# Kernel optimization log

Hardware: AMD Instinct MI355X
Metric: run time of the kernel (lower is better)

Reference implementation:

```python
import jax, jax.numpy as jnp
import numpy as np

EPS = 1e-5


def spline_conv(x, src, dst, pseudo, W, root, bias, num_nodes, K=5):
    """Degree-1 open B-spline conv (torch_spline_conv semantics), mean aggregation.
    W: [kernel_total, Cin, Cout]. kernel_total==1 means trivial basis (kernel_size=1)."""
    E = src.shape[0]
    Cin = x.shape[1]
    KT = W.shape[0]
    x_j = x[src]                                            # [E, Cin] edge gather
    deg = jax.ops.segment_sum(jnp.ones((E,), x.dtype), dst, num_segments=num_nodes)
    deg = jnp.maximum(deg, 1.0)
    if KT == 1:
        agg = jax.ops.segment_sum(x_j, dst, num_segments=num_nodes)
        out = (agg / deg[:, None]) @ W[0]
    else:
        v = pseudo * (K - 1)                                # open spline: v in [0, K-1]
        f = jnp.clip(jnp.floor(v), 0.0, K - 2)
        frac = v - f                                        # [E, 2]
        fi = f.astype(jnp.int32)
        # bucket basis-weighted source features by (kernel_index, dst) then one dense einsum
        h = jnp.zeros((KT * num_nodes, Cin), x.dtype)
        for s0 in (0, 1):
            for s1 in (0, 1):
                b0 = frac[:, 0] if s0 else 1.0 - frac[:, 0]
                b1 = frac[:, 1] if s1 else 1.0 - frac[:, 1]
                basis = b0 * b1                             # [E]
                wi = (fi[:, 0] + s0) + K * (fi[:, 1] + s1)  # [E] kernel index in [0,25)
                seg = wi * num_nodes + dst
                h = h + jax.ops.segment_sum(basis[:, None] * x_j, seg,
                                            num_segments=KT * num_nodes)
        agg = jnp.einsum('knc,kco->no', h.reshape(KT, num_nodes, Cin), W)
        out = agg / deg[:, None]
    return out + x @ root + bias


def batch_norm(x, gamma, beta):
    m = x.mean(axis=0)
    var = jnp.mean((x - m) ** 2, axis=0)
    return gamma * (x - m) * jax.lax.rsqrt(var + EPS) + beta


def setup_inputs() -> dict:
    key = jax.random.key(0)
    ks = jax.random.split(key, 8)
    N, E, Cin, Cout = 50000, 800000, 32, 64
    x = jax.random.normal(ks[0], (N, Cin), jnp.float32)
    edge_index = jax.random.randint(ks[1], (2, E), 0, N, jnp.int32)
    edge_attr = jax.random.uniform(ks[2], (E, 2), jnp.float32)
    s = 0.1
    return {
        'x': x, 'edge_index': edge_index, 'edge_attr': edge_attr,
        'w1': jax.random.normal(ks[3], (25, Cin, Cout), jnp.float32) * s,
        'r1': jax.random.normal(ks[4], (Cin, Cout), jnp.float32) * s,
        'b1': jnp.zeros((Cout,), jnp.float32),
        'g1': jnp.ones((Cout,), jnp.float32),
        'beta1': jnp.zeros((Cout,), jnp.float32),
        'w2': jax.random.normal(ks[5], (25, Cout, Cout), jnp.float32) * s,
        'r2': jax.random.normal(ks[6], (Cout, Cout), jnp.float32) * s,
        'b2': jnp.zeros((Cout,), jnp.float32),
        'g2': jnp.ones((Cout,), jnp.float32),
        'beta2': jnp.zeros((Cout,), jnp.float32),
        'ws': jax.random.normal(ks[7], (1, Cin, Cout), jnp.float32) * s,
        'rs': jax.random.normal(jax.random.fold_in(key, 99), (Cin, Cout), jnp.float32) * s,
        'bs': jnp.zeros((Cout,), jnp.float32),
        'gs': jnp.ones((Cout,), jnp.float32),
        'betas': jnp.zeros((Cout,), jnp.float32),
    }


def reference(x, edge_index, edge_attr, w1, r1, b1, g1, beta1,
              w2, r2, b2, g2, beta2, ws, rs, bs, gs, betas):
    N = x.shape[0]
    src, dst = edge_index[0], edge_index[1]
    h = jax.nn.elu(batch_norm(spline_conv(x, src, dst, edge_attr, w1, r1, b1, N), g1, beta1))
    left = batch_norm(spline_conv(h, src, dst, edge_attr, w2, r2, b2, N), g2, beta2)
    short = batch_norm(spline_conv(x, src, dst, edge_attr, ws, rs, bs, N), gs, betas)
    return jax.nn.elu(left + short)
```

## Files before the change

kernel.cpp:

```cpp
#include <hip/hip_runtime.h>

#define NN 50000
#define NE 800000
#define DBINS 1024

typedef __attribute__((ext_vector_type(8))) short bf16x8;
typedef __attribute__((ext_vector_type(4))) float f32x4;
typedef __attribute__((ext_vector_type(2))) float f32x2;

__device__ __forceinline__ unsigned short f2bf(float f) {
    union { float f; unsigned u; } v; v.f = f;
    unsigned r = v.u + 0x7FFFu + ((v.u >> 16) & 1u);
    return (unsigned short)(r >> 16);
}

__device__ __forceinline__ int4 ld_ep2(const int4* ep, unsigned idx, int which) {
    return *(const int4*)((const char*)ep + (size_t)(idx * 32u + (unsigned)which * 16u));
}
__device__ __forceinline__ unsigned ld_xu(const unsigned* X, unsigned byteoff) {
    return *(const unsigned*)((const char*)X + (size_t)byteoff);
}

__device__ __forceinline__ f32x2 unpack2(unsigned u) {
    union { unsigned u; float f; } a, b;
    a.u = u << 16;
    b.u = u & 0xFFFF0000u;
    return f32x2{a.f, b.f};
}

__device__ __forceinline__ f32x2 pk_mul_hib(f32x2 w, f32x2 x) {
    f32x2 d;
    asm("v_pk_mul_f32 %0, %1, %2 op_sel:[1,0] op_sel_hi:[1,1]"
        : "=v"(d) : "v"(w), "v"(x));
    return d;
}
__device__ __forceinline__ void pk_fma_lob(f32x2& h, f32x2 w, f32x2 t) {
    asm("v_pk_fma_f32 %0, %1, %2, %0 op_sel:[0,0,0] op_sel_hi:[0,1,1]"
        : "+v"(h) : "v"(w), "v"(t));
}

__device__ __forceinline__ int us_idx(int kk, int r, int m) {
    return kk*544 + (r >> 3)*136 + m*8 + (r & 7);
}

template<bool HS>
__device__ __forceinline__ void edge_acc2(f32x2* h, f32x2& hs,
                                          const int4& pa, const int4& pb, f32x2 x) {
    f32x2 wxy[5];
    wxy[0] = unpack2((unsigned)pa.y);
    wxy[1] = unpack2((unsigned)pa.z);
    wxy[2] = unpack2((unsigned)pa.w);
    wxy[3] = unpack2((unsigned)pb.x);
    wxy[4] = unpack2((unsigned)pb.y);
    if (HS) hs += x;
#pragma unroll
    for (int r1 = 0; r1 < 5; ++r1) {
        f32x2 ty = pk_mul_hib(wxy[r1], x);
#pragma unroll
        for (int r0 = 0; r0 < 5; ++r0)
            pk_fma_lob(h[r1*5 + r0], wxy[r0], ty);
    }
}

__device__ __forceinline__ float eh_reduce(f32x2 v, int eh, int stride) {
    float mine  = eh ? v.y : v.x;
    float other = eh ? v.x : v.y;
    return mine + __shfl_xor(other, stride);
}

__global__ __launch_bounds__(256) void k_zero(int* degi, int* cur, float* stats,
                                              int* dcnt, int* dcur,
                                              unsigned* xz, unsigned* hz) {
    int i = blockIdx.x*256 + threadIdx.x;
    int stride = gridDim.x*256;
    for (int j = i; j < NN; j += stride) { degi[j] = 0; cur[j] = 0; }
    if (i < 384) stats[i] = 0.f;
    if (i < DBINS) { dcnt[i] = 0; dcur[i] = 0; }
    if (i < 16) xz[i] = 0u;
    if (i < 32) hz[i] = 0u;
}

__global__ __launch_bounds__(256) void k_hist(const int* __restrict__ dst, int* degi) {
    int e = blockIdx.x*256 + threadIdx.x;
    if (e < NE) atomicAdd(&degi[dst[e]], 1);
}

__global__ __launch_bounds__(256) void k_scan_block(const int* __restrict__ degi,
                                                    int* off, int* bsum) {
    __shared__ int sh[256];
    int t = threadIdx.x;
    int base = blockIdx.x * 1024;
    int v[4]; int s = 0;
#pragma unroll
    for (int j = 0; j < 4; j++) {
        int idx = base + t*4 + j;
        v[j] = (idx < NN) ? ((degi[idx] + 3) & ~3) : 0;
        s += v[j];
    }
    sh[t] = s; __syncthreads();
    for (int ofs = 1; ofs < 256; ofs <<= 1) {
        int x = (t >= ofs) ? sh[t - ofs] : 0;
        __syncthreads();
        sh[t] += x;
        __syncthreads();
    }
    int ex = sh[t] - s;
#pragma unroll
    for (int j = 0; j < 4; j++) {
        int idx = base + t*4 + j;
        if (idx < NN) off[idx] = ex;
        ex += v[j];
    }
    if (t == 255) bsum[blockIdx.x] = sh[255];
}

__global__ __launch_bounds__(256) void k_scan_top(const int* __restrict__ bsum,
                                                  int* bpre, int nb) {
    __shared__ int sh[256];
    int t = threadIdx.x;
    int s = (t < nb) ? bsum[t] : 0;
    sh[t] = s; __syncthreads();
    for (int ofs = 1; ofs < 256; ofs <<= 1) {
        int x = (t >= ofs) ? sh[t - ofs] : 0;
        __syncthreads();
        sh[t] += x;
        __syncthreads();
    }
    if (t < nb) bpre[t] = sh[t] - s;
}

__global__ __launch_bounds__(256) void k_scan_add(int* off, const int* __restrict__ bpre,
                                                  const int* __restrict__ degi) {
    int i = blockIdx.x*256 + threadIdx.x;
    if (i < NN) {
        int v = off[i] + bpre[i >> 10];
        off[i] = v;
        if (i == NN - 1) off[NN] = v + ((degi[i] + 3) & ~3);
    }
}

__global__ __launch_bounds__(256) void k_dhist(const int* __restrict__ degi, int* dcnt) {
    __shared__ int lh[DBINS];
    int t = threadIdx.x;
#pragma unroll
    for (int j = 0; j < DBINS/256; ++j) lh[t + 256*j] = 0;
    __syncthreads();
    int n = blockIdx.x*256 + t;
    if (n < NN) atomicAdd(&lh[min(degi[n], DBINS-1)], 1);
    __syncthreads();
#pragma unroll
    for (int j = 0; j < DBINS/256; ++j) {
        int b = t + 256*j;
        if (lh[b]) atomicAdd(&dcnt[b], lh[b]);
    }
}

__global__ __launch_bounds__(256) void k_dscan(const int* __restrict__ dcnt, int* dbase) {
    __shared__ int sh[256];
    int t = threadIdx.x;
    int v[4]; int s = 0;
#pragma unroll
    for (int j = 0; j < 4; j++) { v[j] = dcnt[t*4 + j]; s += v[j]; }
    sh[t] = s; __syncthreads();
    for (int ofs = 1; ofs < 256; ofs <<= 1) {
        int x = (t >= ofs) ? sh[t - ofs] : 0;
        __syncthreads();
        sh[t] += x;
        __syncthreads();
    }
    int ex = sh[t] - s;
#pragma unroll
    for (int j = 0; j < 4; j++) { dbase[t*4 + j] = ex; ex += v[j]; }
}

__global__ __launch_bounds__(256) void k_pscatter(const int* __restrict__ degi,
                                                  const int* __restrict__ dbase,
                                                  int* dcur, int* perm) {
    __shared__ int lh[DBINS];
    __shared__ int lb[DBINS];
    int t = threadIdx.x;
#pragma unroll
    for (int j = 0; j < DBINS/256; ++j) lh[t + 256*j] = 0;
    __syncthreads();
    int n = blockIdx.x*256 + t;
    int d = 0, lr = 0;
    bool act = (n < NN);
    if (act) {
        d = min(degi[n], DBINS-1);
        lr = atomicAdd(&lh[d], 1);
    }
    __syncthreads();
#pragma unroll
    for (int j = 0; j < DBINS/256; ++j) {
        int b = t + 256*j;
        int c = lh[b];
        lb[b] = c ? atomicAdd(&dcur[b], c) : 0;
    }
    __syncthreads();
    if (act) perm[dbase[d] + lb[d] + lr] = n;
}

__global__ __launch_bounds__(256) void k_scatter(const int* __restrict__ src,
                                                 const int* __restrict__ dst,
                                                 const float* __restrict__ ea,
                                                 const int* __restrict__ off, int* cur,
                                                 int4* __restrict__ ep) {
    int e = blockIdx.x*256 + threadIdx.x;
    if (e >= NE) return;
    int d = dst[e];
    int p = off[d] + atomicAdd(&cur[d], 1);
    float v0 = ea[2*e]     * 4.f;
    float v1 = ea[2*e + 1] * 4.f;
    unsigned w[5];
#pragma unroll
    for (int r = 0; r < 5; ++r) {
        float wx = fmaxf(1.f - fabsf(v0 - (float)r), 0.f);
        float wy = fmaxf(1.f - fabsf(v1 - (float)r), 0.f);
        w[r] = (unsigned)f2bf(wx) | ((unsigned)f2bf(wy) << 16);
    }
    ep[2*p]     = make_int4(src[e], (int)w[0], (int)w[1], (int)w[2]);
    ep[2*p + 1] = make_int4((int)w[3], (int)w[4], 0, 0);
}

__global__ __launch_bounds__(256) void k_pad(const int* __restrict__ off,
                                             const int* __restrict__ degi,
                                             int4* __restrict__ ep) {
    int n = blockIdx.x*256 + threadIdx.x;
    if (n >= NN) return;
    int base = off[n] + degi[n];
    int end  = off[n + 1];
    for (int p = base; p < end; ++p) {
        ep[2*p]     = make_int4(NN, 0, 0, 0);
        ep[2*p + 1] = make_int4(0, 0, 0, 0);
    }
}

__global__ __launch_bounds__(256) void k_xbf(const float* __restrict__ x,
                                             unsigned short* __restrict__ xb) {
    int i = blockIdx.x*256 + threadIdx.x;
    if (i >= NN*8) return;
    float4 v = ((const float4*)x)[i];
    uint2 pk;
    pk.x = (unsigned)f2bf(v.x) | ((unsigned)f2bf(v.y) << 16);
    pk.y = (unsigned)f2bf(v.z) | ((unsigned)f2bf(v.w) << 16);
    ((uint2*)xb)[i] = pk;
}

__global__ __launch_bounds__(256) void k_wprep(const float* __restrict__ W,
                                               const float* __restrict__ root,
                                               int KTC, unsigned short* Wb) {
    int tid = blockIdx.x*256 + threadIdx.x;
    int lane = tid & 63, cot = (tid >> 6) & 3, kk = tid >> 8;
    int co = 16*cot + (lane & 15);
    int kbase = kk*32 + ((lane >> 4) * 8);
    union { unsigned short s[8]; uint4 v; } u;
#pragma unroll
    for (int j = 0; j < 8; j++) {
        int k = kbase + j;
        float val = (k < KTC) ? W[(size_t)k*64 + co] : root[(size_t)(k - KTC)*64 + co];
        u.s[j] = f2bf(val);
    }
    *(uint4*)(Wb + (size_t)tid * 8) = u.v;
}

__global__ __launch_bounds__(512, 4) void k_conv1s(
        const unsigned* __restrict__ Xbf,
        const int* __restrict__ off,
        const int* __restrict__ degi,
        const int4* __restrict__ ep,
        const int* __restrict__ perm,
        const unsigned short* __restrict__ Wb1,
        const unsigned short* __restrict__ WbS,
        const float* __restrict__ b1,
        const float* __restrict__ bs,
        float* __restrict__ agg1,
        float* __restrict__ aggS) {
    __shared__ __align__(16) unsigned short hb[28*544];
    const int t = threadIdx.x;
    const int g = t >> 5;
    const int q = t & 31;
    const int chp = q & 15;
    const int eh = q >> 4;
    const int n0 = blockIdx.x * 16;
    const int n = perm[n0 + g];

    f32x2 h[25], hs = {0.f, 0.f};
#pragma unroll
    for (int i = 0; i < 25; ++i) h[i] = f32x2{0.f, 0.f};

    const int ebeg = off[n], eend = off[n + 1];
    const float rdeg = 1.f / (float)max(degi[n], 1);

    for (int i = ebeg; i < eend; i += 4) {
        const unsigned i0 = (unsigned)(i + eh), i1 = (unsigned)(i + 2 + eh);
        int4 a0 = ld_ep2(ep, i0, 0), b0 = ld_ep2(ep, i0, 1);
        int4 a1 = ld_ep2(ep, i1, 0), b1 = ld_ep2(ep, i1, 1);
        unsigned u0 = ld_xu(Xbf, (unsigned)a0.x * 64u + (unsigned)chp * 4u);
        unsigned u1 = ld_xu(Xbf, (unsigned)a1.x * 64u + (unsigned)chp * 4u);
        edge_acc2<true>(h, hs, a0, b0, unpack2(u0));
        edge_acc2<true>(h, hs, a1, b1, unpack2(u1));
    }

    const int c = 2*chp + eh;
    const int bw = us_idx(0, c, g);
#pragma unroll
    for (int wi = 0; wi < 25; ++wi)
        hb[wi*544 + bw] = f2bf(eh_reduce(h[wi], eh, 16) * rdeg);
    hb[26*544 + bw] = f2bf(eh_reduce(hs, eh, 16) * rdeg);
    {
        unsigned ux = Xbf[(unsigned)n * 16u + (unsigned)chp];
        unsigned short xb = eh ? (unsigned short)(ux >> 16)
                               : (unsigned short)(ux & 0xFFFFu);
        hb[25*544 + bw] = xb;
        hb[27*544 + bw] = xb;
    }
    __syncthreads();

    const int lane = t & 63, w = t >> 6;
    const int m = lane & 15, qq = lane >> 4;
    const int co = (w & 3)*16 + m;
    const int4 pn = ((const int4*)perm)[(n0 >> 2) + qq];
    const int prow[4] = {pn.x, pn.y, pn.z, pn.w};
    if (w < 4) {
        f32x4 acc = {0.f, 0.f, 0.f, 0.f};
        for (int kk = 0; kk < 26; ++kk) {
            bf16x8 av = *(const bf16x8*)&hb[kk*544 + qq*136 + m*8];
            bf16x8 bv = *(const bf16x8*)(Wb1 + (size_t)((kk*4 + w)*64 + lane) * 8);
            acc = __builtin_amdgcn_mfma_f32_16x16x32_bf16(av, bv, acc, 0, 0, 0);
        }
        const float bb = b1[co];
#pragma unroll
        for (int r = 0; r < 4; ++r)
            agg1[(size_t)prow[r]*64 + co] = acc[r] + bb;
    } else {
        f32x4 accs = {0.f, 0.f, 0.f, 0.f};
#pragma unroll
        for (int s = 0; s < 2; ++s) {
            bf16x8 av = *(const bf16x8*)&hb[(26 + s)*544 + qq*136 + m*8];
            bf16x8 bv = *(const bf16x8*)(WbS + (size_t)((s*4 + (w & 3))*64 + lane) * 8);
            accs = __builtin_amdgcn_mfma_f32_16x16x32_bf16(av, bv, accs, 0, 0, 0);
        }
        const float bb = bs[co];
#pragma unroll
        for (int r = 0; r < 4; ++r)
            aggS[(size_t)prow[r]*64 + co] = accs[r] + bb;
    }
}

__global__ __launch_bounds__(512, 4) void k_conv2(
        const unsigned* __restrict__ Xbf,
        const int* __restrict__ off,
        const int* __restrict__ degi,
        const int4* __restrict__ ep,
        const int* __restrict__ perm,
        const unsigned short* __restrict__ Wb2,
        const float* __restrict__ b2,
        float* __restrict__ agg) {
    __shared__ __align__(16) unsigned short hb[52*544];
    const int t = threadIdx.x, lane = t & 63, w = t >> 6;
    const int n0 = blockIdx.x * 16;
    const int chp = lane & 31, eh = lane >> 5;
    const int c = 2*chp + eh;
    const int kh = c >> 5, r = c & 31;

#pragma unroll
    for (int nn = 0; nn < 2; ++nn) {
        const int g = 2*w + nn;
        const int n = perm[n0 + g];
        f32x2 h[25]; f32x2 hsd = {0.f, 0.f};
#pragma unroll
        for (int i = 0; i < 25; ++i) h[i] = f32x2{0.f, 0.f};

        const int ebeg = off[n], eend = off[n + 1];
        const float rdeg = 1.f / (float)max(degi[n], 1);

        for (int i = ebeg; i < eend; i += 4) {
            const unsigned i0 = (unsigned)(i + eh), i1 = (unsigned)(i + 2 + eh);
            int4 a0 = ld_ep2(ep, i0, 0), b0 = ld_ep2(ep, i0, 1);
            int4 a1 = ld_ep2(ep, i1, 0), b1 = ld_ep2(ep, i1, 1);
            unsigned u0 = ld_xu(Xbf, (unsigned)a0.x * 128u + (unsigned)chp * 4u);
            unsigned u1 = ld_xu(Xbf, (unsigned)a1.x * 128u + (unsigned)chp * 4u);
            edge_acc2<false>(h, hsd, a0, b0, unpack2(u0));
            edge_acc2<false>(h, hsd, a1, b1, unpack2(u1));
        }

        const int bw = us_idx(0, r, g);
#pragma unroll
        for (int wi = 0; wi < 25; ++wi)
            hb[(wi*2 + kh)*544 + bw] = f2bf(eh_reduce(h[wi], eh, 32) * rdeg);
        {
            unsigned ux = Xbf[(unsigned)n * 32u + (unsigned)chp];
            hb[(50 + kh)*544 + bw] =
                (unsigned short)(eh ? (ux >> 16) : (ux & 0xFFFFu));
        }
    }
    __syncthreads();

    if (w >= 4) return;

    const int m = lane & 15, qq = lane >> 4;
    const int4 pn = ((const int4*)perm)[(n0 >> 2) + qq];
    const int prow[4] = {pn.x, pn.y, pn.z, pn.w};
    f32x4 acc = {0.f, 0.f, 0.f, 0.f};
    for (int kk = 0; kk < 52; ++kk) {
        bf16x8 av = *(const bf16x8*)&hb[kk*544 + qq*136 + m*8];
        bf16x8 bv = *(const bf16x8*)(Wb2 + (size_t)((kk*4 + w)*64 + lane) * 8);
        acc = __builtin_amdgcn_mfma_f32_16x16x32_bf16(av, bv, acc, 0, 0, 0);
    }
    const int co = w*16 + m;
    const float bb = b2[co];
#pragma unroll
    for (int rr = 0; rr < 4; ++rr)
        agg[(size_t)prow[rr]*64 + co] = acc[rr] + bb;
}

__global__ __launch_bounds__(256) void k_bnstats(const float* __restrict__ agg, float* stats) {
    __shared__ float sh0[256], sh1[256];
    int t = threadIdx.x;
    float s = 0.f, ss = 0.f;
    int stride = gridDim.x * 256;
    for (int i = blockIdx.x*256 + t; i < NN*64; i += stride) {
        float v = agg[i];
        s += v; ss += v*v;
    }
    sh0[t] = s; sh1[t] = ss;
    __syncthreads();
    if (t < 64) {
        float a = sh0[t] + sh0[t+64] + sh0[t+128] + sh0[t+192];
        float b = sh1[t] + sh1[t+64] + sh1[t+128] + sh1[t+192];
        atomicAdd(&stats[t], a);
        atomicAdd(&stats[64 + t], b);
    }
}

__device__ __forceinline__ float eluf(float u) { return u > 0.f ? u : expm1f(u); }

__global__ __launch_bounds__(256) void k_bn_elu(const float* __restrict__ agg,
                                                const float* __restrict__ stats,
                                                const float* __restrict__ gamma,
                                                const float* __restrict__ beta,
                                                unsigned short* __restrict__ outb) {
    int i = blockIdx.x*256 + threadIdx.x;
    if (i >= NN*16) return;
    float4 v = ((const float4*)agg)[i];
    float r[4] = {v.x, v.y, v.z, v.w};
    int c0 = (i << 2) & 63;
#pragma unroll
    for (int j = 0; j < 4; j++) {
        int c = c0 + j;
        float mu = stats[c] * (1.f/NN);
        float var = stats[64 + c] * (1.f/NN) - mu*mu;
        float sc = gamma[c] * rsqrtf(fmaxf(var, 0.f) + 1e-5f);
        r[j] = eluf((r[j] - mu)*sc + beta[c]);
    }
    uint2 pk;
    pk.x = (unsigned)f2bf(r[0]) | ((unsigned)f2bf(r[1]) << 16);
    pk.y = (unsigned)f2bf(r[2]) | ((unsigned)f2bf(r[3]) << 16);
    ((uint2*)outb)[i] = pk;
}

__global__ __launch_bounds__(256) void k_bn_final(const float* __restrict__ a2,
                                                  const float* __restrict__ st2,
                                                  const float* __restrict__ g2,
                                                  const float* __restrict__ be2,
                                                  const float* __restrict__ as,
                                                  const float* __restrict__ sts,
                                                  const float* __restrict__ gs,
                                                  const float* __restrict__ bes,
                                                  float* __restrict__ out) {
    int i = blockIdx.x*256 + threadIdx.x;
    if (i >= NN*16) return;
    float4 v2 = ((const float4*)a2)[i];
    float4 vs = ((const float4*)as)[i];
    float r2v[4] = {v2.x, v2.y, v2.z, v2.w};
    float rsv[4] = {vs.x, vs.y, vs.z, vs.w};
    float o[4];
    int c0 = (i << 2) & 63;
#pragma unroll
    for (int j = 0; j < 4; j++) {
        int c = c0 + j;
        float mu2 = st2[c] * (1.f/NN);
        float var2 = st2[64 + c] * (1.f/NN) - mu2*mu2;
        float sc2 = g2[c] * rsqrtf(fmaxf(var2, 0.f) + 1e-5f);
        float mus = sts[c] * (1.f/NN);
        float vars = sts[64 + c] * (1.f/NN) - mus*mus;
        float scs = gs[c] * rsqrtf(fmaxf(vars, 0.f) + 1e-5f);
        float u = (r2v[j] - mu2)*sc2 + be2[c] + (rsv[j] - mus)*scs + bes[c];
        o[j] = eluf(u);
    }
    ((float4*)out)[i] = make_float4(o[0], o[1], o[2], o[3]);
}

extern "C" void kernel_launch(void* const* d_in, const int* in_sizes, int n_in,
                              void* d_out, int out_size, void* d_ws, size_t ws_size,
                              hipStream_t stream) {
    const float* x   = (const float*)d_in[0];
    const int*   ei  = (const int*)d_in[1];
    const float* ea  = (const float*)d_in[2];
    const float* w1  = (const float*)d_in[3];
    const float* r1  = (const float*)d_in[4];
    const float* b1  = (const float*)d_in[5];
    const float* g1  = (const float*)d_in[6];
    const float* be1 = (const float*)d_in[7];
    const float* w2  = (const float*)d_in[8];
    const float* r2  = (const float*)d_in[9];
    const float* b2  = (const float*)d_in[10];
    const float* g2  = (const float*)d_in[11];
    const float* be2 = (const float*)d_in[12];
    const float* wsN = (const float*)d_in[13];
    const float* rs  = (const float*)d_in[14];
    const float* bs  = (const float*)d_in[15];
    const float* gs  = (const float*)d_in[16];
    const float* bes = (const float*)d_in[17];
    const int* srcp = ei;
    const int* dstp = ei + NE;

    char* wsb = (char*)d_ws;
    size_t o = 0;
    auto alloc = [&](size_t bytes) -> char* {
        char* p = wsb + o;
        o += (bytes + 255) & ~(size_t)255;
        return p;
    };
    int*    degi    = (int*)   alloc((size_t)NN * 4);
    int*    cur     = (int*)   alloc((size_t)NN * 4);
    int*    off     = (int*)   alloc((size_t)(NN + 1) * 4);
    int*    bsum    = (int*)   alloc(256 * 4);
    int*    bpre    = (int*)   alloc(256 * 4);
    int*    dcnt    = (int*)   alloc(DBINS * 4);
    int*    dcur    = (int*)   alloc(DBINS * 4);
    int*    dbase   = (int*)   alloc(DBINS * 4);
    int*    perm    = (int*)   alloc((size_t)NN * 4);
    int4*   ep      = (int4*)  alloc(((size_t)NE + 3*NN + 64) * 32);
    unsigned short* Wb1 = (unsigned short*)alloc(26 * 4096);
    unsigned short* WbS = (unsigned short*)alloc(2 * 4096);
    unsigned short* Wb2 = (unsigned short*)alloc(52 * 4096);
    float*  agg1    = (float*) alloc((size_t)NN * 64 * 4);
    float*  aggS    = (float*) alloc((size_t)NN * 64 * 4);
    unsigned short* h1bf = (unsigned short*)alloc((size_t)(NN + 1) * 64 * 2);
    unsigned short* xbf  = (unsigned short*)alloc((size_t)(NN + 1) * 32 * 2);
    float*  stats   = (float*) alloc(384 * 4);
    (void)ws_size; (void)in_sizes; (void)n_in; (void)out_size;

    float* out = (float*)d_out;

    k_zero<<<196, 256, 0, stream>>>(degi, cur, stats, dcnt, dcur,
                                    (unsigned*)(xbf + (size_t)NN * 32),
                                    (unsigned*)(h1bf + (size_t)NN * 64));
    k_hist<<<3125, 256, 0, stream>>>(dstp, degi);
    k_scan_block<<<49, 256, 0, stream>>>(degi, off, bsum);
    k_scan_top<<<1, 256, 0, stream>>>(bsum, bpre, 49);
    k_scan_add<<<196, 256, 0, stream>>>(off, bpre, degi);
    k_dhist<<<196, 256, 0, stream>>>(degi, dcnt);
    k_dscan<<<1, 256, 0, stream>>>(dcnt, dbase);
    k_pscatter<<<196, 256, 0, stream>>>(degi, dbase, dcur, perm);
    k_scatter<<<3125, 256, 0, stream>>>(srcp, dstp, ea, off, cur, ep);
    k_pad<<<196, 256, 0, stream>>>(off, degi, ep);

    k_xbf<<<1563, 256, 0, stream>>>(x, xbf);
    k_wprep<<<26, 256, 0, stream>>>(w1, r1, 800, Wb1);
    k_wprep<<<2, 256, 0, stream>>>(wsN, rs, 32, WbS);
    k_wprep<<<52, 256, 0, stream>>>(w2, r2, 1600, Wb2);

    k_conv1s<<<3125, 512, 0, stream>>>((const unsigned*)xbf, off, degi, ep, perm,
                                       Wb1, WbS, b1, bs, agg1, aggS);
    k_bnstats<<<256, 256, 0, stream>>>(agg1, stats);
    k_bn_elu<<<3125, 256, 0, stream>>>(agg1, stats, g1, be1, h1bf);

    k_conv2<<<3125, 512, 0, stream>>>((const unsigned*)h1bf, off, degi, ep, perm,
                                      Wb2, b2, agg1);
    k_bnstats<<<256, 256, 0, stream>>>(agg1, stats + 128);
    k_bnstats<<<256, 256, 0, stream>>>(aggS, stats + 256);
    k_bn_final<<<3125, 256, 0, stream>>>(agg1, stats + 128, g2, be2,
                                         aggS, stats + 256, gs, bes, out);
}
```

Baseline: 458.4 us.

## Fuse small prep kernels and shrink conv2 blocks to eight nodes

Cuts the launch count by merging the two top-level scans into one two-block kernel, folding padding into the permutation scatter, combining the x bf16 conversion with all weight prep, and merging the two final BN stat passes. conv2 also moves to 256-thread blocks covering 8 nodes, with a smaller LDS tile and twice as many blocks, to raise occupancy. The MFMA stage in conv2 now computes 16 rows and keeps only 8, so half of that matrix work is wasted.

```diff
diff --git a/kernel.cpp b/kernel.cpp
--- a/kernel.cpp
+++ b/kernel.cpp
@@ -41,6 +41,9 @@
 
 __device__ __forceinline__ int us_idx(int kk, int r, int m) {
     return kk*544 + (r >> 3)*136 + m*8 + (r & 7);
+}
+__device__ __forceinline__ int us8_idx(int kk, int r, int m) {
+    return kk*272 + (r >> 3)*68 + m*8 + (r & 7);
 }
 
 template<bool HS>
@@ -114,19 +117,53 @@
     if (t == 255) bsum[blockIdx.x] = sh[255];
 }
 
-__global__ __launch_bounds__(256) void k_scan_top(const int* __restrict__ bsum,
-                                                  int* bpre, int nb) {
+__global__ __launch_bounds__(256) void k_dhist(const int* __restrict__ degi, int* dcnt) {
+    __shared__ int lh[DBINS];
+    int t = threadIdx.x;
+#pragma unroll
+    for (int j = 0; j < DBINS/256; ++j) lh[t + 256*j] = 0;
+    __syncthreads();
+    int n = blockIdx.x*256 + t;
+    if (n < NN) atomicAdd(&lh[min(degi[n], DBINS-1)], 1);
+    __syncthreads();
+#pragma unroll
+    for (int j = 0; j < DBINS/256; ++j) {
+        int b = t + 256*j;
+        if (lh[b]) atomicAdd(&dcnt[b], lh[b]);
+    }
+}
+
+__global__ __launch_bounds__(256) void k_topscan(const int* __restrict__ bsum,
+                                                 int* bpre, int nb,
+                                                 const int* __restrict__ dcnt,
+                                                 int* dbase) {
     __shared__ int sh[256];
     int t = threadIdx.x;
-    int s = (t < nb) ? bsum[t] : 0;
-    sh[t] = s; __syncthreads();
-    for (int ofs = 1; ofs < 256; ofs <<= 1) {
-        int x = (t >= ofs) ? sh[t - ofs] : 0;
-        __syncthreads();
-        sh[t] += x;
-        __syncthreads();
-    }
-    if (t < nb) bpre[t] = sh[t] - s;
+    if (blockIdx.x == 0) {
+        int s = (t < nb) ? bsum[t] : 0;
+        sh[t] = s; __syncthreads();
+        for (int ofs = 1; ofs < 256; ofs <<= 1) {
+            int x = (t >= ofs) ? sh[t - ofs] : 0;
+            __syncthreads();
+            sh[t] += x;
+            __syncthreads();
+        }
+        if (t < nb) bpre[t] = sh[t] - s;
+    } else {
+        int v[4]; int s = 0;
+#pragma unroll
+        for (int j = 0; j < 4; j++) { v[j] = dcnt[t*4 + j]; s += v[j]; }
+        sh[t] = s; __syncthreads();
+        for (int ofs = 1; ofs < 256; ofs <<= 1) {
+            int x = (t >= ofs) ? sh[t - ofs] : 0;
+            __syncthreads();
+            sh[t] += x;
+            __syncthreads();
+        }
+        int ex = sh[t] - s;
+#pragma unroll
+        for (int j = 0; j < 4; j++) { dbase[t*4 + j] = ex; ex += v[j]; }
+    }
 }
 
 __global__ __launch_bounds__(256) void k_scan_add(int* off, const int* __restrict__ bpre,
@@ -139,43 +176,11 @@
     }
 }
 
-__global__ __launch_bounds__(256) void k_dhist(const int* __restrict__ degi, int* dcnt) {
-    __shared__ int lh[DBINS];
-    int t = threadIdx.x;
-#pragma unroll
-    for (int j = 0; j < DBINS/256; ++j) lh[t + 256*j] = 0;
-    __syncthreads();
-    int n = blockIdx.x*256 + t;
-    if (n < NN) atomicAdd(&lh[min(degi[n], DBINS-1)], 1);
-    __syncthreads();
-#pragma unroll
-    for (int j = 0; j < DBINS/256; ++j) {
-        int b = t + 256*j;
-        if (lh[b]) atomicAdd(&dcnt[b], lh[b]);
-    }
-}
-
-__global__ __launch_bounds__(256) void k_dscan(const int* __restrict__ dcnt, int* dbase) {
-    __shared__ int sh[256];
-    int t = threadIdx.x;
-    int v[4]; int s = 0;
-#pragma unroll
-    for (int j = 0; j < 4; j++) { v[j] = dcnt[t*4 + j]; s += v[j]; }
-    sh[t] = s; __syncthreads();
-    for (int ofs = 1; ofs < 256; ofs <<= 1) {
-        int x = (t >= ofs) ? sh[t - ofs] : 0;
-        __syncthreads();
-        sh[t] += x;
-        __syncthreads();
-    }
-    int ex = sh[t] - s;
-#pragma unroll
-    for (int j = 0; j < 4; j++) { dbase[t*4 + j] = ex; ex += v[j]; }
-}
-
-__global__ __launch_bounds__(256) void k_pscatter(const int* __restrict__ degi,
-                                                  const int* __restrict__ dbase,
-                                                  int* dcur, int* perm) {
+__global__ __launch_bounds__(256) void k_pscatter_pad(const int* __restrict__ degi,
+                                                      const int* __restrict__ dbase,
+                                                      int* dcur, int* perm,
+                                                      const int* __restrict__ off,
+                                                      int4* __restrict__ ep) {
     __shared__ int lh[DBINS];
     __shared__ int lb[DBINS];
     int t = threadIdx.x;
@@ -197,7 +202,15 @@
         lb[b] = c ? atomicAdd(&dcur[b], c) : 0;
     }
     __syncthreads();
-    if (act) perm[dbase[d] + lb[d] + lr] = n;
+    if (act) {
+        perm[dbase[d] + lb[d] + lr] = n;
+        int base = off[n] + degi[n];
+        int end  = off[n + 1];
+        for (int p = base; p < end; ++p) {
+            ep[2*p]     = make_int4(NN, 0, 0, 0);
+            ep[2*p + 1] = make_int4(0, 0, 0, 0);
+        }
+    }
 }
 
 __global__ __launch_bounds__(256) void k_scatter(const int* __restrict__ src,
@@ -222,34 +235,8 @@
     ep[2*p + 1] = make_int4((int)w[3], (int)w[4], 0, 0);
 }
 
-__global__ __launch_bounds__(256) void k_pad(const int* __restrict__ off,
-                                             const int* __restrict__ degi,
-                                             int4* __restrict__ ep) {
-    int n = blockIdx.x*256 + threadIdx.x;
-    if (n >= NN) return;
-    int base = off[n] + degi[n];
-    int end  = off[n + 1];
-    for (int p = base; p < end; ++p) {
-        ep[2*p]     = make_int4(NN, 0, 0, 0);
-        ep[2*p + 1] = make_int4(0, 0, 0, 0);
-    }
-}
-
-__global__ __launch_bounds__(256) void k_xbf(const float* __restrict__ x,
-                                             unsigned short* __restrict__ xb) {
-    int i = blockIdx.x*256 + threadIdx.x;
-    if (i >= NN*8) return;
-    float4 v = ((const float4*)x)[i];
-    uint2 pk;
-    pk.x = (unsigned)f2bf(v.x) | ((unsigned)f2bf(v.y) << 16);
-    pk.y = (unsigned)f2bf(v.z) | ((unsigned)f2bf(v.w) << 16);
-    ((uint2*)xb)[i] = pk;
-}
-
-__global__ __launch_bounds__(256) void k_wprep(const float* __restrict__ W,
-                                               const float* __restrict__ root,
-                                               int KTC, unsigned short* Wb) {
-    int tid = blockIdx.x*256 + threadIdx.x;
+__device__ __forceinline__ void wprep_body(int tid, const float* W, const float* root,
+                                           int KTC, unsigned short* Wb) {
     int lane = tid & 63, cot = (tid >> 6) & 3, kk = tid >> 8;
     int co = 16*cot + (lane & 15);
     int kbase = kk*32 + ((lane >> 4) * 8);
@@ -261,6 +248,35 @@
         u.s[j] = f2bf(val);
     }
     *(uint4*)(Wb + (size_t)tid * 8) = u.v;
+}
+
+__global__ __launch_bounds__(256) void k_prep(const float* __restrict__ x,
+                                              unsigned short* __restrict__ xb,
+                                              const float* __restrict__ w1,
+                                              const float* __restrict__ r1,
+                                              unsigned short* Wb1,
+                                              const float* __restrict__ wsN,
+                                              const float* __restrict__ rs,
+                                              unsigned short* WbS,
+                                              const float* __restrict__ w2,
+                                              const float* __restrict__ r2,
+                                              unsigned short* Wb2) {
+    int b = blockIdx.x, t = threadIdx.x;
+    if (b < 1563) {
+        int i = b*256 + t;
+        if (i >= NN*8) return;
+        float4 v = ((const float4*)x)[i];
+        uint2 pk;
+        pk.x = (unsigned)f2bf(v.x) | ((unsigned)f2bf(v.y) << 16);
+        pk.y = (unsigned)f2bf(v.z) | ((unsigned)f2bf(v.w) << 16);
+        ((uint2*)xb)[i] = pk;
+    } else if (b < 1589) {
+        wprep_body((b - 1563)*256 + t, w1, r1, 800, Wb1);
+    } else if (b < 1591) {
+        wprep_body((b - 1589)*256 + t, wsN, rs, 32, WbS);
+    } else {
+        wprep_body((b - 1591)*256 + t, w2, r2, 1600, Wb2);
+    }
 }
 
 __global__ __launch_bounds__(512, 4) void k_conv1s(
@@ -347,7 +363,7 @@
     }
 }
 
-__global__ __launch_bounds__(512, 4) void k_conv2(
+__global__ __launch_bounds__(256, 5) void k_conv2(
         const unsigned* __restrict__ Xbf,
         const int* __restrict__ off,
         const int* __restrict__ degi,
@@ -356,9 +372,9 @@
         const unsigned short* __restrict__ Wb2,
         const float* __restrict__ b2,
         float* __restrict__ agg) {
-    __shared__ __align__(16) unsigned short hb[52*544];
+    __shared__ __align__(16) unsigned short hb[52*272 + 256];
     const int t = threadIdx.x, lane = t & 63, w = t >> 6;
-    const int n0 = blockIdx.x * 16;
+    const int n0 = blockIdx.x * 8;
     const int chp = lane & 31, eh = lane >> 5;
     const int c = 2*chp + eh;
     const int kh = c >> 5, r = c & 31;
@@ -384,34 +400,34 @@
             edge_acc2<false>(h, hsd, a1, b1, unpack2(u1));
         }
 
-        const int bw = us_idx(0, r, g);
+        const int bw = us8_idx(0, r, g);
 #pragma unroll
         for (int wi = 0; wi < 25; ++wi)
-            hb[(wi*2 + kh)*544 + bw] = f2bf(eh_reduce(h[wi], eh, 32) * rdeg);
+            hb[(wi*2 + kh)*272 + bw] = f2bf(eh_reduce(h[wi], eh, 32) * rdeg);
         {
             unsigned ux = Xbf[(unsigned)n * 32u + (unsigned)chp];
-            hb[(50 + kh)*544 + bw] =
+            hb[(50 + kh)*272 + bw] =
                 (unsigned short)(eh ? (ux >> 16) : (ux & 0xFFFFu));
         }
     }
     __syncthreads();
 
-    if (w >= 4) return;
-
     const int m = lane & 15, qq = lane >> 4;
-    const int4 pn = ((const int4*)perm)[(n0 >> 2) + qq];
-    const int prow[4] = {pn.x, pn.y, pn.z, pn.w};
     f32x4 acc = {0.f, 0.f, 0.f, 0.f};
     for (int kk = 0; kk < 52; ++kk) {
-        bf16x8 av = *(const bf16x8*)&hb[kk*544 + qq*136 + m*8];
+        bf16x8 av = *(const bf16x8*)&hb[kk*272 + qq*68 + m*8];
         bf16x8 bv = *(const bf16x8*)(Wb2 + (size_t)((kk*4 + w)*64 + lane) * 8);
         acc = __builtin_amdgcn_mfma_f32_16x16x32_bf16(av, bv, acc, 0, 0, 0);
     }
-    const int co = w*16 + m;
-    const float bb = b2[co];
-#pragma unroll
-    for (int rr = 0; rr < 4; ++rr)
-        agg[(size_t)prow[rr]*64 + co] = acc[rr] + bb;
+    if (qq < 2) {
+        const int4 pn = ((const int4*)perm)[(n0 >> 2) + qq];
+        const int prow[4] = {pn.x, pn.y, pn.z, pn.w};
+        const int co = w*16 + m;
+        const float bb = b2[co];
+#pragma unroll
+        for (int rr = 0; rr < 4; ++rr)
+            agg[(size_t)prow[rr]*64 + co] = acc[rr] + bb;
+    }
 }
 
 __global__ __launch_bounds__(256) void k_bnstats(const float* __restrict__ agg, float* stats) {
@@ -430,6 +446,29 @@
         float b = sh1[t] + sh1[t+64] + sh1[t+128] + sh1[t+192];
         atomicAdd(&stats[t], a);
         atomicAdd(&stats[64 + t], b);
+    }
+}
+
+__global__ __launch_bounds__(256) void k_bnstats2(const float* __restrict__ a1,
+                                                  const float* __restrict__ as,
+                                                  float* stats) {
+    __shared__ float sh0[256], sh1[256];
+    int t = threadIdx.x;
+    const float* src = (blockIdx.x < 256) ? a1 : as;
+    float* dst = (blockIdx.x < 256) ? (stats + 128) : (stats + 256);
+    int bid = (blockIdx.x < 256) ? blockIdx.x : blockIdx.x - 256;
+    float s = 0.f, ss = 0.f;
+    for (int i = bid*256 + t; i < NN*64; i += 256*256) {
+        float v = src[i];
+        s += v; ss += v*v;
+    }
+    sh0[t] = s; sh1[t] = ss;
+    __syncthreads();
+    if (t < 64) {
+        float a = sh0[t] + sh0[t+64] + sh0[t+128] + sh0[t+192];
+        float b = sh1[t] + sh1[t+64] + sh1[t+128] + sh1[t+192];
+        atomicAdd(&dst[t], a);
+        atomicAdd(&dst[64 + t], b);
     }
 }
 
@@ -549,28 +588,22 @@
                                     (unsigned*)(h1bf + (size_t)NN * 64));
     k_hist<<<3125, 256, 0, stream>>>(dstp, degi);
     k_scan_block<<<49, 256, 0, stream>>>(degi, off, bsum);
-    k_scan_top<<<1, 256, 0, stream>>>(bsum, bpre, 49);
+    k_dhist<<<196, 256, 0, stream>>>(degi, dcnt);
+    k_topscan<<<2, 256, 0, stream>>>(bsum, bpre, 49, dcnt, dbase);
     k_scan_add<<<196, 256, 0, stream>>>(off, bpre, degi);
-    k_dhist<<<196, 256, 0, stream>>>(degi, dcnt);
-    k_dscan<<<1, 256, 0, stream>>>(dcnt, dbase);
-    k_pscatter<<<196, 256, 0, stream>>>(degi, dbase, dcur, perm);
+    k_pscatter_pad<<<196, 256, 0, stream>>>(degi, dbase, dcur, perm, off, ep);
     k_scatter<<<3125, 256, 0, stream>>>(srcp, dstp, ea, off, cur, ep);
-    k_pad<<<196, 256, 0, stream>>>(off, degi, ep);
-
-    k_xbf<<<1563, 256, 0, stream>>>(x, xbf);
-    k_wprep<<<26, 256, 0, stream>>>(w1, r1, 800, Wb1);
-    k_wprep<<<2, 256, 0, stream>>>(wsN, rs, 32, WbS);
-    k_wprep<<<52, 256, 0, stream>>>(w2, r2, 1600, Wb2);
+
+    k_prep<<<1643, 256, 0, stream>>>(x, xbf, w1, r1, Wb1, wsN, rs, WbS, w2, r2, Wb2);
 
     k_conv1s<<<3125, 512, 0, stream>>>((const unsigned*)xbf, off, degi, ep, perm,
                                        Wb1, WbS, b1, bs, agg1, aggS);
     k_bnstats<<<256, 256, 0, stream>>>(agg1, stats);
     k_bn_elu<<<3125, 256, 0, stream>>>(agg1, stats, g1, be1, h1bf);
 
-    k_conv2<<<3125, 512, 0, stream>>>((const unsigned*)h1bf, off, degi, ep, perm,
+    k_conv2<<<6250, 256, 0, stream>>>((const unsigned*)h1bf, off, degi, ep, perm,
                                       Wb2, b2, agg1);
-    k_bnstats<<<256, 256, 0, stream>>>(agg1, stats + 128);
-    k_bnstats<<<256, 256, 0, stream>>>(aggS, stats + 256);
+    k_bnstats2<<<512, 256, 0, stream>>>(agg1, aggS, stats);
     k_bn_final<<<3125, 256, 0, stream>>>(agg1, stats + 128, g2, be2,
                                          aggS, stats + 256, gs, bes, out);
 }
```

Measured after the change: 427.6 us. 1.07x faster.
